# Performance work log

Hardware: AMD Instinct MI355X
Metric: run time of the kernel (lower is better)

## Reference

```python
import jax, jax.numpy as jnp
import numpy as np

B, T, N = 1024, 1024, 32


def setup_inputs() -> dict:
    key = jax.random.key(0)
    k1, k2, k3 = jax.random.split(key, 3)
    logits = jax.random.normal(k1, (B, T, N), dtype=jnp.float32)
    transitions = jax.random.normal(k2, (N, N), dtype=jnp.float32) * 0.1
    sequence_lengths = jax.random.randint(k3, (B,), 0, T, dtype=jnp.int32)
    return {"logits": logits, "transitions": transitions, "sequence_lengths": sequence_lengths}


def reference(logits, transitions, sequence_lengths):
    # Viterbi decode (tfa.text.crf.crf_decode), then mask padding positions to 0.
    Bd, Td, Nd = logits.shape
    tag_ids = jnp.arange(Nd, dtype=jnp.int32)
    init_state = logits[:, 0, :]  # [B, N] viterbi scores at t=0

    def step(state, xs):
        logit_t, t = xs
        # scores[b, prev, cur] = state[b, prev] + transitions[prev, cur]
        scores = state[:, :, None] + transitions[None, :, :]  # [B, N, N]
        bp = jnp.argmax(scores, axis=1).astype(jnp.int32)      # [B, N] best prev tag
        new_state = jnp.max(scores, axis=1) + logit_t          # [B, N]
        valid = (t < sequence_lengths)[:, None]                # step t valid if t <= len-1
        state = jnp.where(valid, new_state, state)             # freeze state past seq end
        bp = jnp.where(valid, bp, tag_ids[None, :])            # identity backptr past end
        return state, bp

    xs = (jnp.swapaxes(logits[:, 1:, :], 0, 1), jnp.arange(1, Td))
    final_state, bps = jax.lax.scan(step, init_state, xs)      # bps: [T-1, B, N]
    last_tag = jnp.argmax(final_state, axis=-1).astype(jnp.int32)  # [B]

    def back(tag, bp):
        prev = jnp.take_along_axis(bp, tag[:, None], axis=1)[:, 0]
        return prev, tag  # emit tag at position i+1, carry tag at position i

    first_tag, later = jax.lax.scan(back, last_tag, bps, reverse=True)
    pred = jnp.concatenate([first_tag[:, None], jnp.swapaxes(later, 0, 1)], axis=1)  # [B, T]
    mask = (jnp.arange(Td)[None, :] < sequence_lengths[:, None]).astype(pred.dtype)
    return pred * mask
```

## Files before the change

kernel.cpp:

```cpp
#include <hip/hip_runtime.h>
#include <stdint.h>

#define T_LEN 1024
#define NSTATE 32

typedef int v2i __attribute__((ext_vector_type(2)));

__device__ __forceinline__ float max3f(float a, float b, float c) {
    return fmaxf(fmaxf(a, b), c);
}
__device__ __forceinline__ int min3i(int a, int b, int c) {
    return min(min(a, b), c);
}

__launch_bounds__(64)
__global__ void viterbi_kernel(const float* __restrict__ logits,
                               const float* __restrict__ trans,
                               const int* __restrict__ seqlen,
                               int* __restrict__ out)
{
    const int lane = threadIdx.x;
    const int half = lane >> 5;
    const int j    = lane & 31;
    const int h16  = half * 16;

    __shared__ __align__(16) float st[NSTATE];
    __shared__ uint8_t bp[T_LEN * NSTATE];
    __shared__ uint8_t Farr[NSTATE * NSTATE];
    __shared__ uint8_t earr[NSTATE];
    __shared__ __align__(16) int pred[T_LEN];

    int L = seqlen[blockIdx.x];
    L = min(max(L, 0), T_LEN);

    float tr[16];
#pragma unroll
    for (int k = 0; k < 16; ++k)
        tr[k] = trans[(h16 + k) * NSTATE + j];

    const float* lg = logits + (size_t)blockIdx.x * T_LEN * NSTATE;

    float ns = lg[j];

    st[j] = ns;
    const float4* stv = reinterpret_cast<const float4*>(st) + half * 4;
    float4 q0 = stv[0], q1 = stv[1], q2 = stv[2], q3 = stv[3];

    auto step = [&](int t, float lgt) {
        float v[16];
        v[0]=q0.x+tr[0];  v[1]=q0.y+tr[1];  v[2]=q0.z+tr[2];  v[3]=q0.w+tr[3];
        v[4]=q1.x+tr[4];  v[5]=q1.y+tr[5];  v[6]=q1.z+tr[6];  v[7]=q1.w+tr[7];
        v[8]=q2.x+tr[8];  v[9]=q2.y+tr[9];  v[10]=q2.z+tr[10];v[11]=q2.w+tr[11];
        v[12]=q3.x+tr[12];v[13]=q3.y+tr[13];v[14]=q3.z+tr[14];v[15]=q3.w+tr[15];

        float a0 = max3f(v[0],  v[1],  v[2]);
        float a1 = max3f(v[3],  v[4],  v[5]);
        float a2 = max3f(v[6],  v[7],  v[8]);
        float a3 = max3f(v[9],  v[10], v[11]);
        float a4 = max3f(v[12], v[13], v[14]);
        float b0 = max3f(a0, a1, a2);
        float b1 = max3f(a3, a4, v[15]);
        float hm = fmaxf(b0, b1);

        v2i sw = __builtin_amdgcn_permlane32_swap(__float_as_int(hm),
                                                  __float_as_int(hm), false, false);
        float gm = fmaxf(hm, fmaxf(__int_as_float(sw[0]), __int_as_float(sw[1])));

        ns = gm + lgt;

        st[j] = ns;
        q0 = stv[0]; q1 = stv[1]; q2 = stv[2]; q3 = stv[3];

        int ix[16];
#pragma unroll
        for (int k = 0; k < 16; ++k)
            ix[k] = (v[k] == gm) ? (h16 + k) : 64;
        int c0 = min3i(ix[0],  ix[1],  ix[2]);
        int c1 = min3i(ix[3],  ix[4],  ix[5]);
        int c2 = min3i(ix[6],  ix[7],  ix[8]);
        int c3 = min3i(ix[9],  ix[10], ix[11]);
        int c4 = min3i(ix[12], ix[13], ix[14]);
        int d0 = min3i(c0, c1, c2);
        int d1 = min3i(c3, c4, ix[15]);
        int ih = min(d0, d1);
        v2i swi = __builtin_amdgcn_permlane32_swap(ih, ih, false, false);
        int idx = min3i(ih, swi[0], swi[1]);

        bp[t * NSTATE + j] = (uint8_t)idx;
    };

    if (L >= 2) {
        float pre[8];
#pragma unroll
        for (int d = 0; d < 8; ++d) {
            int tp = 1 + d; if (tp > 1023) tp = 1023;
            pre[d] = lg[tp * NSTATE + j];
        }
        int t = 1;
        for (; t + 8 <= L; t += 8) {
#pragma unroll
            for (int u = 0; u < 8; ++u) {
                step(t + u, pre[u]);
                int tp = t + 8 + u; if (tp > 1023) tp = 1023;
                pre[u] = lg[tp * NSTATE + j];
            }
        }
        for (int k = 0; t < L; ++t, ++k) step(t, pre[k]);
    }

    float m = ns;
#pragma unroll
    for (int d = 1; d < 64; d <<= 1) m = fmaxf(m, __shfl_xor(m, d));
    int ii = (ns == m) ? j : 64;
#pragma unroll
    for (int d = 1; d < 64; d <<= 1) ii = min(ii, __shfl_xor(ii, d));
    const int ft = ii;

    __syncthreads();

    {
        const int c = lane & 31;
        const int j0base = (lane >> 5) * 16;
        int tags[16];
#pragma unroll
        for (int k = 0; k < 16; ++k) tags[k] = j0base + k;
        const int thi = c * 32 + 31;
        for (int s = 0; s < 32; ++s) {
            int t = thi - s;
            bool valid = (t >= 1) && (t <= L - 1);
            int tc = min(max(t, 1), max(L - 1, 1));
            int base = tc * NSTATE;
#pragma unroll
            for (int k = 0; k < 16; ++k) {
                int nt = bp[base + tags[k]];
                tags[k] = valid ? nt : tags[k];
            }
        }
#pragma unroll
        for (int k = 0; k < 16; ++k)
            Farr[c * 32 + j0base + k] = (uint8_t)tags[k];
    }
    __syncthreads();

    if (lane == 0) {
        int e = ft;
        for (int c2 = 31; c2 >= 0; --c2) {
            earr[c2] = (uint8_t)e;
            e = Farr[c2 * 32 + e];
        }
    }
    __syncthreads();

    if (lane < 32) {
        int tag = earr[lane];
        const int thi3 = lane * 32 + 31;
        for (int s = 0; s < 32; ++s) {
            int t = thi3 - s;
            pred[t] = (t < L) ? tag : 0;
            bool valid = (t >= 1) && (t <= L - 1);
            int tc = min(max(t, 1), max(L - 1, 1));
            int nt = bp[tc * NSTATE + tag];
            tag = valid ? nt : tag;
        }
    }
    __syncthreads();

    int4* out4 = reinterpret_cast<int4*>(out + (size_t)blockIdx.x * T_LEN);
    const int4* p4 = reinterpret_cast<const int4*>(pred);
#pragma unroll
    for (int r = 0; r < 4; ++r)
        out4[r * 64 + lane] = p4[r * 64 + lane];
}

extern "C" void kernel_launch(void* const* d_in, const int* in_sizes, int n_in,
                              void* d_out, int out_size, void* d_ws, size_t ws_size,
                              hipStream_t stream) {
    const float* logits = (const float*)d_in[0];
    const float* trans  = (const float*)d_in[1];
    const int*   slen   = (const int*)d_in[2];
    int*         out    = (int*)d_out;
    const int B = in_sizes[2];

    viterbi_kernel<<<dim3(B), dim3(64), 0, stream>>>(logits, trans, slen, out);
}
```

Measured before the change: 250.7 us.

## Software-pipeline Viterbi forward loop, overlapping argmax of step t-1 with max chain

Splits each forward step into a critical-path max/state-update chain and a backpointer argmax. The argmax for the previous step is interleaved with the max chain of the current step, using two alternating score buffers. This exposes instruction-level parallelism in the latency-bound recurrence. The remainder loop is replaced by padded, predicated steps (an active flag freezes the state) with clamped backpointer writes, so a few redundant steps are computed per sequence and register pressure rises from holding two score arrays.

```diff
diff --git a/kernel.cpp b/kernel.cpp
--- a/kernel.cpp
+++ b/kernel.cpp
@@ -46,35 +46,38 @@
     const float4* stv = reinterpret_cast<const float4*>(st) + half * 4;
     float4 q0 = stv[0], q1 = stv[1], q2 = stv[2], q3 = stv[3];
 
-    auto step = [&](int t, float lgt) {
-        float v[16];
-        v[0]=q0.x+tr[0];  v[1]=q0.y+tr[1];  v[2]=q0.z+tr[2];  v[3]=q0.w+tr[3];
-        v[4]=q1.x+tr[4];  v[5]=q1.y+tr[5];  v[6]=q1.z+tr[6];  v[7]=q1.w+tr[7];
-        v[8]=q2.x+tr[8];  v[9]=q2.y+tr[9];  v[10]=q2.z+tr[10];v[11]=q2.w+tr[11];
-        v[12]=q3.x+tr[12];v[13]=q3.y+tr[13];v[14]=q3.z+tr[14];v[15]=q3.w+tr[15];
-
-        float a0 = max3f(v[0],  v[1],  v[2]);
-        float a1 = max3f(v[3],  v[4],  v[5]);
-        float a2 = max3f(v[6],  v[7],  v[8]);
-        float a3 = max3f(v[9],  v[10], v[11]);
-        float a4 = max3f(v[12], v[13], v[14]);
+    auto chain = [&](float lgt, bool act, float (&vo)[16], float& gmo) {
+        vo[0]=q0.x+tr[0];  vo[1]=q0.y+tr[1];  vo[2]=q0.z+tr[2];  vo[3]=q0.w+tr[3];
+        vo[4]=q1.x+tr[4];  vo[5]=q1.y+tr[5];  vo[6]=q1.z+tr[6];  vo[7]=q1.w+tr[7];
+        vo[8]=q2.x+tr[8];  vo[9]=q2.y+tr[9];  vo[10]=q2.z+tr[10];vo[11]=q2.w+tr[11];
+        vo[12]=q3.x+tr[12];vo[13]=q3.y+tr[13];vo[14]=q3.z+tr[14];vo[15]=q3.w+tr[15];
+
+        float a0 = max3f(vo[0],  vo[1],  vo[2]);
+        float a1 = max3f(vo[3],  vo[4],  vo[5]);
+        float a2 = max3f(vo[6],  vo[7],  vo[8]);
+        float a3 = max3f(vo[9],  vo[10], vo[11]);
+        float a4 = max3f(vo[12], vo[13], vo[14]);
         float b0 = max3f(a0, a1, a2);
-        float b1 = max3f(a3, a4, v[15]);
+        float b1 = max3f(a3, a4, vo[15]);
         float hm = fmaxf(b0, b1);
 
         v2i sw = __builtin_amdgcn_permlane32_swap(__float_as_int(hm),
                                                   __float_as_int(hm), false, false);
         float gm = fmaxf(hm, fmaxf(__int_as_float(sw[0]), __int_as_float(sw[1])));
-
-        ns = gm + lgt;
+        gmo = gm;
+
+        float nsn = gm + lgt;
+        ns = act ? nsn : ns;
 
         st[j] = ns;
         q0 = stv[0]; q1 = stv[1]; q2 = stv[2]; q3 = stv[3];
-
+    };
+
+    auto amax = [&](int t, const float (&vi)[16], float gmi) {
         int ix[16];
 #pragma unroll
         for (int k = 0; k < 16; ++k)
-            ix[k] = (v[k] == gm) ? (h16 + k) : 64;
+            ix[k] = (vi[k] == gmi) ? (h16 + k) : 64;
         int c0 = min3i(ix[0],  ix[1],  ix[2]);
         int c1 = min3i(ix[3],  ix[4],  ix[5]);
         int c2 = min3i(ix[6],  ix[7],  ix[8]);
@@ -86,32 +89,49 @@
         v2i swi = __builtin_amdgcn_permlane32_swap(ih, ih, false, false);
         int idx = min3i(ih, swi[0], swi[1]);
 
-        bp[t * NSTATE + j] = (uint8_t)idx;
+        bp[min(t, 1023) * NSTATE + j] = (uint8_t)idx;
     };
 
     if (L >= 2) {
+        float vX[16], vY[16];
+        float gmX, gmY;
+
+        float lg1 = lg[NSTATE + j];
+        chain(lg1, true, vY, gmY);
+
         float pre[8];
 #pragma unroll
-        for (int d = 0; d < 8; ++d) {
-            int tp = 1 + d; if (tp > 1023) tp = 1023;
-            pre[d] = lg[tp * NSTATE + j];
-        }
-        int t = 1;
-        for (; t + 8 <= L; t += 8) {
-#pragma unroll
-            for (int u = 0; u < 8; ++u) {
-                step(t + u, pre[u]);
-                int tp = t + 8 + u; if (tp > 1023) tp = 1023;
-                pre[u] = lg[tp * NSTATE + j];
-            }
-        }
-        for (int k = 0; t < L; ++t, ++k) step(t, pre[k]);
-    }
-
-    float m = ns;
-#pragma unroll
-    for (int d = 1; d < 64; d <<= 1) m = fmaxf(m, __shfl_xor(m, d));
-    int ii = (ns == m) ? j : 64;
+        for (int u = 0; u < 8; ++u)
+            pre[u] = lg[min(2 + u, 1023) * NSTATE + j];
+
+        const int m = L - 2;
+        const int M = (m + 7) & ~7;
+
+        for (int t = 2; t < 2 + M; t += 8) {
+            chain(pre[0], (t+0) < L, vX, gmX); amax(t-1, vY, gmY);
+            pre[0] = lg[min(t+8,  1023) * NSTATE + j];
+            chain(pre[1], (t+1) < L, vY, gmY); amax(t+0, vX, gmX);
+            pre[1] = lg[min(t+9,  1023) * NSTATE + j];
+            chain(pre[2], (t+2) < L, vX, gmX); amax(t+1, vY, gmY);
+            pre[2] = lg[min(t+10, 1023) * NSTATE + j];
+            chain(pre[3], (t+3) < L, vY, gmY); amax(t+2, vX, gmX);
+            pre[3] = lg[min(t+11, 1023) * NSTATE + j];
+            chain(pre[4], (t+4) < L, vX, gmX); amax(t+3, vY, gmY);
+            pre[4] = lg[min(t+12, 1023) * NSTATE + j];
+            chain(pre[5], (t+5) < L, vY, gmY); amax(t+4, vX, gmX);
+            pre[5] = lg[min(t+13, 1023) * NSTATE + j];
+            chain(pre[6], (t+6) < L, vX, gmX); amax(t+5, vY, gmY);
+            pre[6] = lg[min(t+14, 1023) * NSTATE + j];
+            chain(pre[7], (t+7) < L, vY, gmY); amax(t+6, vX, gmX);
+            pre[7] = lg[min(t+15, 1023) * NSTATE + j];
+        }
+        amax(1 + M, vY, gmY);
+    }
+
+    float m2 = ns;
+#pragma unroll
+    for (int d = 1; d < 64; d <<= 1) m2 = fmaxf(m2, __shfl_xor(m2, d));
+    int ii = (ns == m2) ? j : 64;
 #pragma unroll
     for (int d = 1; d < 64; d <<= 1) ii = min(ii, __shfl_xor(ii, d));
     const int ft = ii;
```

Result: slower. 270.5 us (+7.9%).

## Split Viterbi forward pass into max-producer and argmax-consumer wavefronts

Applied to the files above, without the earlier changes.

The block grows to two wavefronts. Wave 0 runs only the max recurrence and publishes each step's state into a 32-slot shared ring with per-slot flags. Wave 1 spins on those flags, recomputes the scores and writes the argmax backpointers, which takes the argmax work off the serial critical path. The cost is spin-wait synchronisation through volatile shared memory, a producer throttle based on the consumer's progress, recomputed adds, and twice the threads per block.

```diff
diff --git a/kernel.cpp b/kernel.cpp
--- a/kernel.cpp
+++ b/kernel.cpp
@@ -3,6 +3,7 @@
 
 #define T_LEN 1024
 #define NSTATE 32
+#define RING 32
 
 typedef int v2i __attribute__((ext_vector_type(2)));
 
@@ -13,22 +14,31 @@
     return min(min(a, b), c);
 }
 
-__launch_bounds__(64)
+__launch_bounds__(128)
 __global__ void viterbi_kernel(const float* __restrict__ logits,
                                const float* __restrict__ trans,
                                const int* __restrict__ seqlen,
                                int* __restrict__ out)
 {
-    const int lane = threadIdx.x;
+    const int tid  = threadIdx.x;
+    const int wid  = tid >> 6;
+    const int lane = tid & 63;
     const int half = lane >> 5;
     const int j    = lane & 31;
     const int h16  = half * 16;
 
-    __shared__ __align__(16) float st[NSTATE];
     __shared__ uint8_t bp[T_LEN * NSTATE];
+    __shared__ __align__(16) char ovl[RING * NSTATE * 4];
     __shared__ uint8_t Farr[NSTATE * NSTATE];
     __shared__ uint8_t earr[NSTATE];
-    __shared__ __align__(16) int pred[T_LEN];
+    __shared__ volatile int flag[RING];
+    __shared__ volatile int hp;
+
+    float (*st_ring)[NSTATE] = (float (*)[NSTATE])ovl;
+    int* pred = (int*)ovl;
+
+    if (tid < RING) flag[tid] = -1;
+    if (tid == 0) hp = 0;
 
     int L = seqlen[blockIdx.x];
     L = min(max(L, 0), T_LEN);
@@ -42,83 +52,126 @@
 
     float ns = lg[j];
 
-    st[j] = ns;
-    const float4* stv = reinterpret_cast<const float4*>(st) + half * 4;
-    float4 q0 = stv[0], q1 = stv[1], q2 = stv[2], q3 = stv[3];
-
-    auto step = [&](int t, float lgt) {
-        float v[16];
-        v[0]=q0.x+tr[0];  v[1]=q0.y+tr[1];  v[2]=q0.z+tr[2];  v[3]=q0.w+tr[3];
-        v[4]=q1.x+tr[4];  v[5]=q1.y+tr[5];  v[6]=q1.z+tr[6];  v[7]=q1.w+tr[7];
-        v[8]=q2.x+tr[8];  v[9]=q2.y+tr[9];  v[10]=q2.z+tr[10];v[11]=q2.w+tr[11];
-        v[12]=q3.x+tr[12];v[13]=q3.y+tr[13];v[14]=q3.z+tr[14];v[15]=q3.w+tr[15];
-
-        float a0 = max3f(v[0],  v[1],  v[2]);
-        float a1 = max3f(v[3],  v[4],  v[5]);
-        float a2 = max3f(v[6],  v[7],  v[8]);
-        float a3 = max3f(v[9],  v[10], v[11]);
-        float a4 = max3f(v[12], v[13], v[14]);
-        float b0 = max3f(a0, a1, a2);
-        float b1 = max3f(a3, a4, v[15]);
-        float hm = fmaxf(b0, b1);
-
-        v2i sw = __builtin_amdgcn_permlane32_swap(__float_as_int(hm),
-                                                  __float_as_int(hm), false, false);
-        float gm = fmaxf(hm, fmaxf(__int_as_float(sw[0]), __int_as_float(sw[1])));
-
-        ns = gm + lgt;
-
-        st[j] = ns;
-        q0 = stv[0]; q1 = stv[1]; q2 = stv[2]; q3 = stv[3];
-
-        int ix[16];
-#pragma unroll
-        for (int k = 0; k < 16; ++k)
-            ix[k] = (v[k] == gm) ? (h16 + k) : 64;
-        int c0 = min3i(ix[0],  ix[1],  ix[2]);
-        int c1 = min3i(ix[3],  ix[4],  ix[5]);
-        int c2 = min3i(ix[6],  ix[7],  ix[8]);
-        int c3 = min3i(ix[9],  ix[10], ix[11]);
-        int c4 = min3i(ix[12], ix[13], ix[14]);
-        int d0 = min3i(c0, c1, c2);
-        int d1 = min3i(c3, c4, ix[15]);
-        int ih = min(d0, d1);
-        v2i swi = __builtin_amdgcn_permlane32_swap(ih, ih, false, false);
-        int idx = min3i(ih, swi[0], swi[1]);
-
-        bp[t * NSTATE + j] = (uint8_t)idx;
-    };
-
-    if (L >= 2) {
-        float pre[8];
-#pragma unroll
-        for (int d = 0; d < 8; ++d) {
-            int tp = 1 + d; if (tp > 1023) tp = 1023;
-            pre[d] = lg[tp * NSTATE + j];
-        }
-        int t = 1;
-        for (; t + 8 <= L; t += 8) {
-#pragma unroll
-            for (int u = 0; u < 8; ++u) {
-                step(t + u, pre[u]);
-                int tp = t + 8 + u; if (tp > 1023) tp = 1023;
-                pre[u] = lg[tp * NSTATE + j];
+    __syncthreads();
+
+    int ft = 0;
+
+    if (wid == 0) {
+        st_ring[0][j] = ns;
+        __asm__ __volatile__("" ::: "memory");
+        flag[0] = 0;
+
+        float4 q0, q1, q2, q3;
+        {
+            const float4* sv = (const float4*)(st_ring[0]) + half * 4;
+            q0 = sv[0]; q1 = sv[1]; q2 = sv[2]; q3 = sv[3];
+        }
+
+        auto mstep = [&](int t, float lgt) {
+            float a0 = max3f(q0.x + tr[0],  q0.y + tr[1],  q0.z + tr[2]);
+            float a1 = max3f(q0.w + tr[3],  q1.x + tr[4],  q1.y + tr[5]);
+            float a2 = max3f(q1.z + tr[6],  q1.w + tr[7],  q2.x + tr[8]);
+            float a3 = max3f(q2.y + tr[9],  q2.z + tr[10], q2.w + tr[11]);
+            float a4 = max3f(q3.x + tr[12], q3.y + tr[13], q3.z + tr[14]);
+            float b0 = max3f(a0, a1, a2);
+            float b1 = max3f(a3, a4, q3.w + tr[15]);
+            float hm = fmaxf(b0, b1);
+
+            v2i sw = __builtin_amdgcn_permlane32_swap(__float_as_int(hm),
+                                                      __float_as_int(hm), false, false);
+            float gm = fmaxf(hm, fmaxf(__int_as_float(sw[0]), __int_as_float(sw[1])));
+
+            ns = gm + lgt;
+
+            if ((t & 7) == 0) { while (t - hp > 16) {} }
+
+            int slot = t & (RING - 1);
+            st_ring[slot][j] = ns;
+            __asm__ __volatile__("" ::: "memory");
+            flag[slot] = t;
+
+            const float4* sv = (const float4*)(st_ring[slot]) + half * 4;
+            q0 = sv[0]; q1 = sv[1]; q2 = sv[2]; q3 = sv[3];
+        };
+
+        if (L >= 2) {
+            float pre[8];
+#pragma unroll
+            for (int d = 0; d < 8; ++d)
+                pre[d] = lg[min(1 + d, T_LEN - 1) * NSTATE + j];
+            int t = 1;
+            for (; t + 8 <= L; t += 8) {
+#pragma unroll
+                for (int u = 0; u < 8; ++u) {
+                    mstep(t + u, pre[u]);
+                    pre[u] = lg[min(t + 8 + u, T_LEN - 1) * NSTATE + j];
+                }
             }
-        }
-        for (int k = 0; t < L; ++t, ++k) step(t, pre[k]);
-    }
-
-    float m = ns;
-#pragma unroll
-    for (int d = 1; d < 64; d <<= 1) m = fmaxf(m, __shfl_xor(m, d));
-    int ii = (ns == m) ? j : 64;
-#pragma unroll
-    for (int d = 1; d < 64; d <<= 1) ii = min(ii, __shfl_xor(ii, d));
-    const int ft = ii;
-
-    __syncthreads();
-
-    {
+            for (int k2 = 0; t < L; ++t, ++k2) mstep(t, pre[k2]);
+        }
+
+        float m2 = ns;
+#pragma unroll
+        for (int d = 1; d < 64; d <<= 1) m2 = fmaxf(m2, __shfl_xor(m2, d));
+        int ii = (ns == m2) ? j : 64;
+#pragma unroll
+        for (int d = 1; d < 64; d <<= 1) ii = min(ii, __shfl_xor(ii, d));
+        ft = ii;
+    } else {
+        if (L >= 2) {
+            for (int t = 1; t < L; ++t) {
+                const int tS = t - 1;
+                const int slot = tS & (RING - 1);
+                while (flag[slot] < tS) {}
+                __asm__ __volatile__("" ::: "memory");
+
+                const float4* sv = (const float4*)(st_ring[slot]) + half * 4;
+                float4 q0 = sv[0], q1 = sv[1], q2 = sv[2], q3 = sv[3];
+
+                float v[16];
+                v[0]=q0.x+tr[0];  v[1]=q0.y+tr[1];  v[2]=q0.z+tr[2];  v[3]=q0.w+tr[3];
+                v[4]=q1.x+tr[4];  v[5]=q1.y+tr[5];  v[6]=q1.z+tr[6];  v[7]=q1.w+tr[7];
+                v[8]=q2.x+tr[8];  v[9]=q2.y+tr[9];  v[10]=q2.z+tr[10];v[11]=q2.w+tr[11];
+                v[12]=q3.x+tr[12];v[13]=q3.y+tr[13];v[14]=q3.z+tr[14];v[15]=q3.w+tr[15];
+
+                float a0 = max3f(v[0],  v[1],  v[2]);
+                float a1 = max3f(v[3],  v[4],  v[5]);
+                float a2 = max3f(v[6],  v[7],  v[8]);
+                float a3 = max3f(v[9],  v[10], v[11]);
+                float a4 = max3f(v[12], v[13], v[14]);
+                float b0 = max3f(a0, a1, a2);
+                float b1 = max3f(a3, a4, v[15]);
+                float hm = fmaxf(b0, b1);
+                v2i sw = __builtin_amdgcn_permlane32_swap(__float_as_int(hm),
+                                                          __float_as_int(hm), false, false);
+                float gm = fmaxf(hm, fmaxf(__int_as_float(sw[0]), __int_as_float(sw[1])));
+
+                int ix[16];
+#pragma unroll
+                for (int k = 0; k < 16; ++k)
+                    ix[k] = (v[k] == gm) ? (h16 + k) : 64;
+                int c0 = min3i(ix[0],  ix[1],  ix[2]);
+                int c1 = min3i(ix[3],  ix[4],  ix[5]);
+                int c2 = min3i(ix[6],  ix[7],  ix[8]);
+                int c3 = min3i(ix[9],  ix[10], ix[11]);
+                int c4 = min3i(ix[12], ix[13], ix[14]);
+                int d0 = min3i(c0, c1, c2);
+                int d1 = min3i(c3, c4, ix[15]);
+                int ih = min(d0, d1);
+                v2i swi = __builtin_amdgcn_permlane32_swap(ih, ih, false, false);
+                int idx = min3i(ih, swi[0], swi[1]);
+
+                bp[t * NSTATE + j] = (uint8_t)idx;
+
+                if ((t & 15) == 0) hp = t;
+            }
+            hp = T_LEN;
+        }
+    }
+
+    __syncthreads();
+
+    if (wid == 0) {
         const int c = lane & 31;
         const int j0base = (lane >> 5) * 16;
         int tags[16];
@@ -142,7 +195,7 @@
     }
     __syncthreads();
 
-    if (lane == 0) {
+    if (tid == 0) {
         int e = ft;
         for (int c2 = 31; c2 >= 0; --c2) {
             earr[c2] = (uint8_t)e;
@@ -151,7 +204,7 @@
     }
     __syncthreads();
 
-    if (lane < 32) {
+    if (wid == 0 && lane < 32) {
         int tag = earr[lane];
         const int thi3 = lane * 32 + 31;
         for (int s = 0; s < 32; ++s) {
@@ -165,11 +218,13 @@
     }
     __syncthreads();
 
-    int4* out4 = reinterpret_cast<int4*>(out + (size_t)blockIdx.x * T_LEN);
-    const int4* p4 = reinterpret_cast<const int4*>(pred);
-#pragma unroll
-    for (int r = 0; r < 4; ++r)
-        out4[r * 64 + lane] = p4[r * 64 + lane];
+    if (wid == 0) {
+        int4* out4 = reinterpret_cast<int4*>(out + (size_t)blockIdx.x * T_LEN);
+        const int4* p4 = reinterpret_cast<const int4*>(pred);
+#pragma unroll
+        for (int r = 0; r < 4; ++r)
+            out4[r * 64 + lane] = p4[r * 64 + lane];
+    }
 }
 
 extern "C" void kernel_launch(void* const* d_in, const int* in_sizes, int n_in,
@@ -181,5 +236,5 @@
     int*         out    = (int*)d_out;
     const int B = in_sizes[2];
 
-    viterbi_kernel<<<dim3(B), dim3(64), 0, stream>>>(logits, trans, slen, out);
-}
+    viterbi_kernel<<<dim3(B), dim3(128), 0, stream>>>(logits, trans, slen, out);
+}
```

Result: slower. 350.8 us (+39.9%).
